# Performance work log

Measured on AMD Instinct MI355X. Metric: run time of the kernel, lower is better.

## Reference

```python
import jax, jax.numpy as jnp
import numpy as np

B, L, C = 8, 3136, 384
H_, W_ = 56, 56
WS, SS, NH = 7, 3, 12
HID, AD, SD = 1536, 16, 48  # mlp hidden, Bi_direct adapter dim, dim//scale_factor


def _rpi(w):
    # relative position index, [N, N] int
    coords = np.stack(np.meshgrid(np.arange(w), np.arange(w), indexing='ij')).reshape(2, -1)
    rc = (coords[:, :, None] - coords[:, None, :]).transpose(1, 2, 0)
    rc[:, :, 0] += w - 1
    rc[:, :, 1] += w - 1
    rc[:, :, 0] *= 2 * w - 1
    return rc.sum(-1)


def _shift_mask(Hp, Wp, w, s):
    # [nW, N, N] float mask with 0 / -100, as in the torch code
    img = np.zeros((1, Hp, Wp, 1), np.float32)
    cnt = 0
    sl = (slice(0, -w), slice(-w, -s), slice(-s, None))
    for h in sl:
        for v in sl:
            img[:, h, v, :] = cnt
            cnt += 1
    mw = img.reshape(1, Hp // w, w, Wp // w, w, 1).transpose(0, 1, 3, 2, 4, 5).reshape(-1, w * w)
    am = mw[:, None, :] - mw[:, :, None]
    return np.where(am != 0, np.float32(-100.0), np.float32(0.0))


def _ln(x, g, b, eps=1e-5):
    m = x.mean(-1, keepdims=True)
    v = ((x - m) ** 2).mean(-1, keepdims=True)
    return (x - m) * jax.lax.rsqrt(v + eps) * g + b


def _wpart(x, w):
    b, h, ww, c = x.shape
    return x.reshape(b, h // w, w, ww // w, w, c).transpose(0, 1, 3, 2, 4, 5).reshape(-1, w, w, c)


def _wrev(win, w, h, ww):
    b = win.shape[0] // (h * ww // w // w)
    return win.reshape(b, h // w, ww // w, w, w, -1).transpose(0, 1, 3, 2, 4, 5).reshape(b, h, ww, -1)


def _attn(xw, w_qkv, b_qkv, w_proj, b_proj, rpb, rpi, mask):
    B_, N, c = xw.shape
    d = c // NH
    scale = d ** -0.5
    qkv = (xw @ w_qkv + b_qkv).reshape(B_, N, 3, NH, d).transpose(2, 0, 3, 1, 4)
    q, k, v = qkv[0] * scale, qkv[1], qkv[2]  # [B_, NH, N, d]
    a = jnp.einsum('bhnd,bhmd->bhnm', q, k)
    bias = rpb[rpi.reshape(-1)].reshape(N, N, NH).transpose(2, 0, 1)
    a = a + bias[None]
    if mask is not None:
        nW = mask.shape[0]
        a = (a.reshape(B_ // nW, nW, NH, N, N) + mask[None, :, None]).reshape(B_, NH, N, N)
    a = jax.nn.softmax(a, axis=-1)
    out = jnp.einsum('bhnm,bhmd->bhnd', a, v).transpose(0, 2, 1, 3).reshape(B_, N, c)
    return out @ w_proj + b_proj


def setup_inputs() -> dict:
    key = jax.random.key(0)
    ks = iter(jax.random.split(key, 24))
    r = lambda shape: jax.random.normal(next(ks), shape, jnp.float32) * 0.02
    inp = dict(
        x_FMAG=jax.random.normal(next(ks), (B, L, C), jnp.float32),
        x=jax.random.normal(next(ks), (B, L, C), jnp.float32),
        z=jax.random.normal(next(ks), (B, L, C), jnp.float32),
        mask_z=1,
        ln1_g=jnp.ones(C), ln1_b=jnp.zeros(C),
        ln2_g=jnp.ones(C), ln2_b=jnp.zeros(C),
        w_qkv=r((C, 3 * C)), b_qkv=jnp.zeros(3 * C),
        w_proj=r((C, C)), b_proj=jnp.zeros(C),
        rpb=r(((2 * WS - 1) ** 2, NH)),
        w_fc1=r((C, HID)), b_fc1=jnp.zeros(HID),
        w_fc2=r((HID, C)), b_fc2=jnp.zeros(C),
        st_dw=r((C, SD)), st_db=jnp.zeros(SD), st_uw=r((SD, C)), st_ub=jnp.zeros(C),
        t_dw=r((C, AD)), t_db=jnp.zeros(AD), t_uw=r((AD, C)), t_ub=jnp.zeros(C),
        t2_dw=r((C, AD)), t2_db=jnp.zeros(AD), t2_uw=r((AD, C)), t2_ub=jnp.zeros(C),
    )
    return inp


def reference(x_FMAG, x, z, mask_z, ln1_g, ln1_b, ln2_g, ln2_b, w_qkv, b_qkv, w_proj, b_proj, rpb,
              w_fc1, b_fc1, w_fc2, b_fc2, st_dw, st_db, st_uw, st_ub,
              t_dw, t_db, t_uw, t_ub, t2_dw, t2_db, t2_uw, t2_ub):
    rpi = jnp.asarray(_rpi(WS))
    gelu = lambda y: jax.nn.gelu(y, approximate=False)
    # adapter_st (Single_adapter_s): bottleneck with GELU
    x = gelu(x_FMAG @ st_dw + st_db) @ st_uw + st_ub + x
    shortcut_x = x
    xn = _ln(x, ln1_g, ln1_b).reshape(B, H_, W_, C)
    # x branch: NO pre-shift (faithful to source), no mask, but rolled +shift after
    xw = _wpart(xn, WS).reshape(-1, WS * WS, C)
    awx = _attn(xw, w_qkv, b_qkv, w_proj, b_proj, rpb, rpi, None)
    awx4 = awx.reshape(-1, WS, WS, C)
    x = jnp.roll(_wrev(awx4, WS, H_, W_), (SS, SS), (1, 2)).reshape(B, L, C)
    # z branch: shifted, with shift attention mask (mask_z is not None)
    shortcut_z = z
    zn = _ln(z, ln1_g, ln1_b).reshape(B, H_, W_, C)
    sz = jnp.roll(zn, (-SS, -SS), (1, 2))
    mask = jnp.asarray(_shift_mask(H_, W_, WS, SS)) if mask_z else None
    zw = _wpart(sz, WS).reshape(-1, WS * WS, C)
    awz = _attn(zw, w_qkv, b_qkv, w_proj, b_proj, rpb, rpi, mask)
    awz4 = awz.reshape(-1, WS, WS, C)
    z = jnp.roll(_wrev(awz4, WS, H_, W_), (SS, SS), (1, 2)).reshape(B, L, C)
    # cross adapters (Bi_direct_adapter: linear down/up, no activation)
    ad_t = lambda y: (y @ t_dw + t_db) @ t_uw + t_ub
    ad_t2 = lambda y: (y @ t2_dw + t2_db) @ t2_uw + t2_ub
    x1 = shortcut_x + x + ad_t(shortcut_z)
    z1 = shortcut_z + z + ad_t(shortcut_x)
    mlp = lambda y: gelu(y @ w_fc1 + b_fc1) @ w_fc2 + b_fc2
    x2 = x1 + mlp(_ln(x1, ln2_g, ln2_b)) + ad_t2(z1)
    z2 = z1 + mlp(_ln(z1, ln2_g, ln2_b)) + ad_t2(x1)
    return (x2, awx4, z2, awz4)
```

## Files before the change

### kernel.cpp

```cpp
#include <hip/hip_runtime.h>
#include <hip/hip_bf16.h>


#define TOK 25088
#define TELEM 9633792L

typedef __attribute__((ext_vector_type(4))) float f32x4;
typedef __attribute__((ext_vector_type(8))) short bf16x8;
typedef __attribute__((address_space(3))) unsigned int as3_u32;
typedef __attribute__((address_space(1))) const unsigned int as1_u32;

__device__ __forceinline__ float ldc(const void* p, long i, int code, int bf) {
  if (code == 1 ? bf : (code == 2))
    return __bfloat162float(((const __hip_bfloat16*)p)[i]);
  return ((const float*)p)[i];
}
__device__ __forceinline__ void stAny(void* p, long i, int bf, float v) {
  if (bf) ((__hip_bfloat16*)p)[i] = __float2bfloat16(v);
  else ((float*)p)[i] = v;
}
__device__ __forceinline__ unsigned short f2b(float f) {
  __hip_bfloat16 h = __float2bfloat16(f);
  return *reinterpret_cast<unsigned short*>(&h);
}
__device__ __forceinline__ void ld8f(const void* p, long rowbase, int c,
                                     int code, int bf, float* o) {
  bool isb = (code == 1) ? (bf != 0) : (code == 2);
  if (isb) {
    bf16x8 v = *(const bf16x8*)((const __hip_bfloat16*)p + rowbase + c);
#pragma unroll
    for (int i = 0; i < 8; ++i)
      o[i] = __uint_as_float(((unsigned int)(unsigned short)v[i]) << 16);
  } else {
    const float* f = (const float*)p + rowbase + c;
#pragma unroll
    for (int i = 0; i < 8; ++i) o[i] = f[i];
  }
}
__device__ __forceinline__ void st8(void* p, long rowbase, int c, bool isb,
                                    const float* o) {
  if (isb) {
    bf16x8 v;
#pragma unroll
    for (int i = 0; i < 8; ++i) v[i] = (short)f2b(o[i]);
    *(bf16x8*)((__hip_bfloat16*)p + rowbase + c) = v;
  } else {
    float* f = (float*)p + rowbase + c;
#pragma unroll
    for (int i = 0; i < 8; ++i) f[i] = o[i];
  }
}

__global__ void detect_dtype(const unsigned int* __restrict__ w, int* flag) {
  __shared__ int cnt;
  if (threadIdx.x == 0) cnt = 0;
  __syncthreads();
  int local = 0;
  for (int i = threadIdx.x; i < 4096; i += blockDim.x) {
    unsigned int lo = w[i] & 0xFFFFu;
    unsigned int e = (lo >> 7) & 0xFFu;
    if ((e >= 100u && e <= 135u) || lo == 0u) local++;
  }
  atomicAdd(&cnt, local);
  __syncthreads();
  if (threadIdx.x == 0) *flag = (cnt > 2600) ? 1 : 0;
}

__global__ __launch_bounds__(256) void transpose_to_bf16(
    const void* __restrict__ in, __hip_bfloat16* __restrict__ out, int K,
    int N, const int* __restrict__ flagp) {
  int bf = *flagp;
  __shared__ float tile[32][33];
  int nb = blockIdx.x * 32, kb = blockIdx.y * 32;
  int tx = threadIdx.x & 31, ty = threadIdx.x >> 5;
#pragma unroll
  for (int r = 0; r < 32; r += 8)
    tile[ty + r][tx] = ldc(in, (long)(kb + ty + r) * N + nb + tx, 1, bf);
  __syncthreads();
#pragma unroll
  for (int r = 0; r < 32; r += 8)
    out[(long)(nb + ty + r) * K + kb + tx] = __float2bfloat16(tile[tx][ty + r]);
}

__global__ __launch_bounds__(256) void build_tab(const void* __restrict__ rpb,
                                                 float* __restrict__ tab,
                                                 const int* __restrict__ flagp) {
  int bf = *flagp;
  int idx = blockIdx.x * 256 + threadIdx.x;
  if (idx >= 48 * 2401) return;
  int m = idx % 49;
  int n = (idx / 49) % 49;
  int head = (idx / 2401) % 12;
  int cls = idx / (2401 * 12);
  int in_ = n / 7, jn = n % 7, im = m / 7, jm = m % 7;
  int ridx = (in_ - im + 6) * 13 + (jn - jm + 6);
  float v = ldc(rpb, (long)ridx * 12 + head, 1, bf);
  int whE = (cls >> 1) & 1, wwE = cls & 1;
  int rhn = whE ? (in_ < 4 ? 1 : 2) : 0;
  int rwn = wwE ? (jn < 4 ? 1 : 2) : 0;
  int rhm = whE ? (im < 4 ? 1 : 2) : 0;
  int rwm = wwE ? (jm < 4 ? 1 : 2) : 0;
  if ((rhn * 3 + rwn) != (rhm * 3 + rwm)) v -= 100.f;
  tab[idx] = v;
}

__global__ __launch_bounds__(512) void gemm_bf16(
    const __hip_bfloat16* __restrict__ A, const __hip_bfloat16* __restrict__ BT,
    const void* __restrict__ bias, void* __restrict__ C, int cmode, long coff,
    long coff2, long Msplit, int accum, int doGelu, int M, int N, int K,
    const int* __restrict__ flagp) {
  const int bf = *flagp;
  __shared__ __hip_bfloat16 As[2][256 * 32];
  __shared__ __hip_bfloat16 Bs[2][128 * 32];
  const int tid = threadIdx.x;
  const int lane = tid & 63, wave = tid >> 6;
  const int wr = wave >> 1, wc = wave & 1;

  const int gx = gridDim.x;
  long id = (long)blockIdx.y * gx + blockIdx.x;
  const long nwg = (long)gx * gridDim.y;
  {
    const long q = nwg >> 3, r = nwg & 7;
    const long xcd = id & 7, pos = id >> 3;
    id = (xcd < r) ? xcd * (q + 1) + pos : r * (q + 1) + (xcd - r) * q + pos;
  }
  const long m0 = (id / gx) * 256;
  const int n0 = (int)(id % gx) * 128;

  f32x4 acc[4][4] = {};

  const int srow = wave * 16 + (lane >> 2);
  const int scol = (lane & 3) * 8;
  const __hip_bfloat16* pA0 = A + (m0 + srow) * K + scol;
  const __hip_bfloat16* pB0 = BT + (long)(n0 + srow) * K + scol;
  const long rstepA = 128 * (long)K;
  const int ldsA0 = (wave * 16) * 32;
  const int ldsA1 = (128 + wave * 16) * 32;
  const int ldsB0 = (wave * 16) * 32;

  const int row = lane & 15;
  const int kk = (lane >> 4) * 8;
  const int nt = K / 32;

  auto stage = [&](int buf, int t) {
    const int k0 = t * 32;
    __builtin_amdgcn_global_load_lds((as1_u32*)(pA0 + k0),
                                     (as3_u32*)(&As[buf][ldsA0]), 16, 0, 0);
    __builtin_amdgcn_global_load_lds((as1_u32*)(pA0 + rstepA + k0),
                                     (as3_u32*)(&As[buf][ldsA1]), 16, 0, 0);
    __builtin_amdgcn_global_load_lds((as1_u32*)(pB0 + k0),
                                     (as3_u32*)(&Bs[buf][ldsB0]), 16, 0, 0);
  };

  stage(0, 0);
  if (nt > 1) {
    stage(1, 1);
    asm volatile("s_waitcnt vmcnt(3)" ::: "memory");
  } else {
    asm volatile("s_waitcnt vmcnt(0)" ::: "memory");
  }
  __builtin_amdgcn_sched_barrier(0);
  __builtin_amdgcn_s_barrier();

  for (int t = 0; t < nt; ++t) {
    const int cur = t & 1;
    bf16x8 af[4], bfr[4];
#pragma unroll
    for (int i = 0; i < 4; ++i)
      af[i] = *(const bf16x8*)(&As[cur][(wr * 64 + i * 16 + row) * 32 + kk]);
#pragma unroll
    for (int j = 0; j < 4; ++j)
      bfr[j] = *(const bf16x8*)(&Bs[cur][(wc * 64 + j * 16 + row) * 32 + kk]);
    asm volatile("s_waitcnt lgkmcnt(0)" ::: "memory");
    __builtin_amdgcn_sched_barrier(0);
    __builtin_amdgcn_s_barrier();
    if (t + 2 < nt) stage(cur, t + 2);
#pragma unroll
    for (int i = 0; i < 4; ++i)
#pragma unroll
      for (int j = 0; j < 4; ++j)
        acc[i][j] = __builtin_amdgcn_mfma_f32_16x16x32_bf16(af[i], bfr[j],
                                                            acc[i][j], 0, 0, 0);
    if (t + 1 < nt) {
      if (t + 2 < nt)
        asm volatile("s_waitcnt vmcnt(3)" ::: "memory");
      else
        asm volatile("s_waitcnt vmcnt(0)" ::: "memory");
      __builtin_amdgcn_sched_barrier(0);
      __builtin_amdgcn_s_barrier();
    }
  }

  const int crow = (lane >> 4) * 4;
  const int ccol = lane & 15;
#pragma unroll
  for (int i = 0; i < 4; ++i) {
#pragma unroll
    for (int r = 0; r < 4; ++r) {
      long m = m0 + wr * 64 + i * 16 + crow + r;
#pragma unroll
      for (int j = 0; j < 4; ++j) {
        int n = n0 + wc * 64 + j * 16 + ccol;
        float v = acc[i][j][r];
        if (bias) v += ldc(bias, n, 1, bf);
        if (doGelu) v = 0.5f * v * (1.f + erff(v * 0.70710678118f));
        long idx = m * (long)N + n;
        if (cmode == 0) {
          ((__hip_bfloat16*)C)[idx] = __float2bfloat16(v);
        } else {
          long odx = (m < Msplit) ? coff + idx
                                  : coff2 + (m - Msplit) * (long)N + n;
          if (accum) v += ldc(C, odx, 1, bf);
          stAny(C, odx, bf, v);
        }
      }
    }
  }
}

__global__ __launch_bounds__(256) void st_fused(
    const void* __restrict__ xF, const void* __restrict__ x_in,
    const void* __restrict__ dw, const void* __restrict__ db,
    const void* __restrict__ uw, const void* __restrict__ ub,
    __hip_bfloat16* __restrict__ out, const int* __restrict__ flagp) {
  const int bf = *flagp;
  __shared__ float Wd[48 * 384];
  __shared__ float Wu[48 * 384];
  __shared__ float Db[48], Ub[384];
  for (int i = threadIdx.x; i < 48 * 384; i += 256) {
    int k = i / 384, c = i % 384;
    Wd[i] = ldc(dw, (long)c * 48 + k, 1, bf);
    Wu[i] = ldc(uw, i, 1, bf);
  }
  for (int i = threadIdx.x; i < 48; i += 256) Db[i] = ldc(db, i, 1, bf);
  for (int i = threadIdx.x; i < 384; i += 256) Ub[i] = ldc(ub, i, 1, bf);
  __syncthreads();
  const long t = (long)blockIdx.x * 256 + threadIdx.x;
  float hid[48];
#pragma unroll
  for (int k = 0; k < 48; ++k) hid[k] = Db[k];
  for (int c = 0; c < 384; c += 8) {
    float x8[8];
    ld8f(xF, t * 384, c, 1, bf, x8);
    for (int k = 0; k < 48; ++k) {
      const float* w = &Wd[k * 384 + c];
      float s = 0.f;
#pragma unroll
      for (int i = 0; i < 8; ++i) s += x8[i] * w[i];
      hid[k] += s;
    }
  }
#pragma unroll
  for (int k = 0; k < 48; ++k) {
    float h = hid[k];
    hid[k] = 0.5f * h * (1.f + erff(h * 0.70710678118f));
  }
  for (int c = 0; c < 384; c += 8) {
    float o[8];
    ld8f(x_in, t * 384, c, 1, bf, o);
#pragma unroll
    for (int i = 0; i < 8; ++i) o[i] += Ub[c + i];
    for (int k = 0; k < 48; ++k) {
      const float* w = &Wu[k * 384 + c];
      float h = hid[k];
#pragma unroll
      for (int i = 0; i < 8; ++i) o[i] += h * w[i];
    }
    st8(out, t * 384, c, true, o);
  }
}

__global__ __launch_bounds__(256) void adapter_dual(
    const void* __restrict__ inA, int cA, const void* __restrict__ inB, int cB,
    const void* __restrict__ baseX, int cbX, const void* __restrict__ baseZ,
    int cbZ, const void* __restrict__ gat, long goffX, long goffZ,
    int doGather, const void* __restrict__ dw, const void* __restrict__ dbias,
    const void* __restrict__ uw, const void* __restrict__ ubias,
    void* __restrict__ outX, long ooffX, void* __restrict__ outZ, long ooffZ,
    int outRaw, const int* __restrict__ flagp) {
  const int bf = *flagp;
  __shared__ float Wd[16 * 384];
  __shared__ float Wu[16 * 384];
  __shared__ float Db[16], Ub[384];
  for (int i = threadIdx.x; i < 16 * 384; i += 256) {
    int k = i / 384, c = i % 384;
    Wd[i] = ldc(dw, (long)c * 16 + k, 1, bf);
    Wu[i] = ldc(uw, i, 1, bf);
  }
  if (threadIdx.x < 16) Db[threadIdx.x] = ldc(dbias, threadIdx.x, 1, bf);
  for (int i = threadIdx.x; i < 384; i += 256) Ub[i] = ldc(ubias, i, 1, bf);
  __syncthreads();
  const long t = (long)blockIdx.x * 256 + threadIdx.x;
  long grow = 0;
  if (doGather) {
    int b = (int)(t / 3136);
    int hw = (int)(t % 3136);
    int h = hw / 56, w = hw % 56;
    int hp = (h - 3 + 56) % 56, wp = (w - 3 + 56) % 56;
    int win = b * 64 + (hp / 7) * 8 + (wp / 7);
    int n = (hp % 7) * 7 + (wp % 7);
    grow = ((long)win * 49 + n) * 384;
  }
  float hidA[16], hidB[16];
#pragma unroll
  for (int k = 0; k < 16; ++k) {
    hidA[k] = Db[k];
    hidB[k] = Db[k];
  }
  for (int c = 0; c < 384; c += 8) {
    float a8[8], b8[8];
    ld8f(inA, t * 384, c, cA, bf, a8);
    ld8f(inB, t * 384, c, cB, bf, b8);
#pragma unroll
    for (int k = 0; k < 16; ++k) {
      const float* w = &Wd[k * 384 + c];
      float sa = 0.f, sb = 0.f;
#pragma unroll
      for (int i = 0; i < 8; ++i) {
        sa += a8[i] * w[i];
        sb += b8[i] * w[i];
      }
      hidA[k] += sa;
      hidB[k] += sb;
    }
  }
  const bool oisb = outRaw ? (bf != 0) : true;
  for (int c = 0; c < 384; c += 8) {
    float ox[8], oz[8];
    ld8f(baseX, t * 384, c, cbX, bf, ox);
    ld8f(baseZ, t * 384, c, cbZ, bf, oz);
    if (doGather) {
      float g[8];
      ld8f(gat, goffX + grow, c, 1, bf, g);
#pragma unroll
      for (int i = 0; i < 8; ++i) ox[i] += g[i];
      ld8f(gat, goffZ + grow, c, 1, bf, g);
#pragma unroll
      for (int i = 0; i < 8; ++i) oz[i] += g[i];
    }
#pragma unroll
    for (int i = 0; i < 8; ++i) {
      ox[i] += Ub[c + i];
      oz[i] += Ub[c + i];
    }
#pragma unroll
    for (int k = 0; k < 16; ++k) {
      const float* w = &Wu[k * 384 + c];
      float ha = hidA[k], hb = hidB[k];
#pragma unroll
      for (int i = 0; i < 8; ++i) {
        ox[i] += ha * w[i];
        oz[i] += hb * w[i];
      }
    }
    st8(outX, ooffX + t * 384, c, oisb, ox);
    st8(outZ, ooffZ + t * 384, c, oisb, oz);
  }
}

__global__ __launch_bounds__(128) void ln_kernel(
    const void* __restrict__ X, int xc, const void* __restrict__ g,
    const void* __restrict__ b, __hip_bfloat16* __restrict__ out,
    const int* __restrict__ flagp) {
  int bf = *flagp;
  long t = blockIdx.x;
  int tid = threadIdx.x;
  float v[3];
  float s = 0.f;
#pragma unroll
  for (int r = 0; r < 3; ++r) {
    v[r] = ldc(X, t * 384 + tid + r * 128, xc, bf);
    s += v[r];
  }
  __shared__ float red[2], red2[2];
  for (int off = 32; off; off >>= 1) s += __shfl_down(s, off, 64);
  if ((tid & 63) == 0) red[tid >> 6] = s;
  __syncthreads();
  float mean = (red[0] + red[1]) * (1.f / 384.f);
  float var = 0.f;
#pragma unroll
  for (int r = 0; r < 3; ++r) {
    float d = v[r] - mean;
    var += d * d;
  }
  for (int off = 32; off; off >>= 1) var += __shfl_down(var, off, 64);
  if ((tid & 63) == 0) red2[tid >> 6] = var;
  __syncthreads();
  float rstd = rsqrtf((red2[0] + red2[1]) * (1.f / 384.f) + 1e-5f);
#pragma unroll
  for (int r = 0; r < 3; ++r) {
    int c = tid + r * 128;
    out[t * 384 + c] = __float2bfloat16((v[r] - mean) * rstd *
                                        ldc(g, c, 1, bf) + ldc(b, c, 1, bf));
  }
}

__global__ __launch_bounds__(256) void attn_mfma(
    const __hip_bfloat16* __restrict__ qkv, const float* __restrict__ tab,
    __hip_bfloat16* __restrict__ outp, const int* __restrict__ maskz) {
  __shared__ __hip_bfloat16 lds[4][64 * 72 + 32 * 72];
  const int wave = threadIdx.x >> 6, lane = threadIdx.x & 63;
  const int pair = blockIdx.x * 4 + wave;
  const int head = pair % 12;
  const int win = pair / 12;
  const int shifted = win >= 512;
  const int wn = win & 511;
  const int b = wn >> 6, wh = (wn >> 3) & 7, ww = wn & 7;
  const int useMask = shifted && (*maskz != 0);
  const int cls = useMask ? (((wh == 7) ? 2 : 0) | ((ww == 7) ? 1 : 0)) : 0;
  const float* tb = tab + (long)(cls * 12 + head) * 2401;
  __hip_bfloat16* P = lds[wave];
  __hip_bfloat16* VT = lds[wave] + 64 * 72;

  auto tokOf = [&](int n) -> long {
    n = (n < 49) ? n : 0;
    int i = n / 7, j = n % 7;
    int h = wh * 7 + i, w = ww * 7 + j;
    if (shifted) {
      h = (h + 3) % 56;
      w = (w + 3) % 56;
    }
    return (shifted ? (long)TOK : 0) + ((long)b * 56 + h) * 56 + w;
  };

  const int fr = lane & 15;
  const int fq = lane >> 4;
  bf16x8 qf[4], kf[4];
#pragma unroll
  for (int i = 0; i < 4; ++i) {
    long t = tokOf(i * 16 + fr);
    const __hip_bfloat16* basep = qkv + t * 1152 + head * 32 + fq * 8;
    qf[i] = *(const bf16x8*)(basep);
    kf[i] = *(const bf16x8*)(basep + 384);
  }
  for (int e = lane; e < 32 * 16; e += 64)
    VT[(e >> 4) * 72 + 48 + (e & 15)] = __float2bfloat16(0.f);
  for (int e = lane; e < 49 * 32; e += 64) {
    int n = e >> 5, d = e & 31;
    VT[d * 72 + n] = qkv[tokOf(n) * 1152 + 768 + head * 32 + d];
  }
  f32x4 acc[4][4] = {};
#pragma unroll
  for (int i = 0; i < 4; ++i)
#pragma unroll
    for (int j = 0; j < 4; ++j)
      acc[i][j] =
          __builtin_amdgcn_mfma_f32_16x16x32_bf16(qf[i], kf[j], acc[i][j], 0, 0, 0);
  const float scale = 0.17677669529663687f;
#pragma unroll
  for (int i = 0; i < 4; ++i) {
#pragma unroll
    for (int r = 0; r < 4; ++r) {
      int n = i * 16 + fq * 4 + r;
      float s[4];
      float mx = -1e30f;
#pragma unroll
      for (int j = 0; j < 4; ++j) {
        int m = j * 16 + fr;
        float v = acc[i][j][r] * scale;
        if (m < 49 && n < 49) v += tb[n * 49 + m];
        s[j] = (m < 49) ? v : -1e30f;
        mx = fmaxf(mx, s[j]);
      }
#pragma unroll
      for (int d = 1; d < 16; d <<= 1) mx = fmaxf(mx, __shfl_xor(mx, d));
      float sum = 0.f;
#pragma unroll
      for (int j = 0; j < 4; ++j) {
        float p = (16 * j + fr < 49) ? __expf(s[j] - mx) : 0.f;
        s[j] = p;
        sum += p;
      }
#pragma unroll
      for (int d = 1; d < 16; d <<= 1) sum += __shfl_xor(sum, d);
      float inv = 1.f / sum;
#pragma unroll
      for (int j = 0; j < 4; ++j)
        P[n * 72 + j * 16 + fr] = __float2bfloat16(s[j] * inv);
    }
  }
  f32x4 o[4][2] = {};
#pragma unroll
  for (int ks = 0; ks < 2; ++ks) {
    bf16x8 pa[4], vb[2];
#pragma unroll
    for (int i2 = 0; i2 < 4; ++i2)
      pa[i2] = *(const bf16x8*)(P + (i2 * 16 + fr) * 72 + ks * 32 + fq * 8);
#pragma unroll
    for (int j2 = 0; j2 < 2; ++j2)
      vb[j2] = *(const bf16x8*)(VT + (j2 * 16 + fr) * 72 + ks * 32 + fq * 8);
#pragma unroll
    for (int i2 = 0; i2 < 4; ++i2)
#pragma unroll
      for (int j2 = 0; j2 < 2; ++j2)
        o[i2][j2] =
            __builtin_amdgcn_mfma_f32_16x16x32_bf16(pa[i2], vb[j2], o[i2][j2], 0, 0, 0);
  }
#pragma unroll
  for (int i2 = 0; i2 < 4; ++i2) {
#pragma unroll
    for (int r = 0; r < 4; ++r) {
      int n = i2 * 16 + fq * 4 + r;
      if (n < 49) {
#pragma unroll
        for (int j2 = 0; j2 < 2; ++j2)
          outp[((long)win * 49 + n) * 384 + head * 32 + j2 * 16 + fr] =
              __float2bfloat16(o[i2][j2][r]);
      }
    }
  }
}

extern "C" void kernel_launch(void* const* d_in, const int* in_sizes, int n_in,
                              void* d_out, int out_size, void* d_ws,
                              size_t ws_size, hipStream_t stream) {
  const void* x_FMAG = d_in[0];
  const void* x_in = d_in[1];
  const void* z_in = d_in[2];
  const int* mask_z = (const int*)d_in[3];
  const void* ln1_g = d_in[4];
  const void* ln1_b = d_in[5];
  const void* ln2_g = d_in[6];
  const void* ln2_b = d_in[7];
  const void* w_qkv = d_in[8];
  const void* b_qkv = d_in[9];
  const void* w_proj = d_in[10];
  const void* b_proj = d_in[11];
  const void* rpb = d_in[12];
  const void* w_fc1 = d_in[13];
  const void* b_fc1 = d_in[14];
  const void* w_fc2 = d_in[15];
  const void* b_fc2 = d_in[16];
  const void* st_dw = d_in[17];
  const void* st_db = d_in[18];
  const void* st_uw = d_in[19];
  const void* st_ub = d_in[20];
  const void* t_dw = d_in[21];
  const void* t_db = d_in[22];
  const void* t_uw = d_in[23];
  const void* t_ub = d_in[24];
  const void* t2_dw = d_in[25];
  const void* t2_db = d_in[26];
  const void* t2_uw = d_in[27];
  const void* t2_ub = d_in[28];

  const long T = TELEM;
  char* base = (char*)d_ws;
  __hip_bfloat16* W6bf = (__hip_bfloat16*)base; base += T * 2;
  __hip_bfloat16* W7bf = (__hip_bfloat16*)base; base += T * 2;
  __hip_bfloat16* Sbf = (__hip_bfloat16*)base; base += 2 * T * 2;
  char* D = base; base += 16 * T;
  __hip_bfloat16* W0bf = (__hip_bfloat16*)D;
  __hip_bfloat16* QKVbf = (__hip_bfloat16*)(D + 2 * T);
  __hip_bfloat16* Hbf = (__hip_bfloat16*)D;
  __hip_bfloat16* TQ = (__hip_bfloat16*)base; base += 384L * 1152 * 2;
  __hip_bfloat16* TP = (__hip_bfloat16*)base; base += 384L * 384 * 2;
  __hip_bfloat16* T1 = (__hip_bfloat16*)base; base += 384L * 1536 * 2;
  __hip_bfloat16* T2 = (__hip_bfloat16*)base; base += 1536L * 384 * 2;
  float* tab = (float*)base; base += 48L * 2401 * 4;
  int* flag = (int*)base;

  detect_dtype<<<1, 256, 0, stream>>>((const unsigned int*)x_FMAG, flag);

  transpose_to_bf16<<<dim3(1152 / 32, 384 / 32), 256, 0, stream>>>(
      w_qkv, TQ, 384, 1152, flag);
  transpose_to_bf16<<<dim3(384 / 32, 384 / 32), 256, 0, stream>>>(
      w_proj, TP, 384, 384, flag);
  transpose_to_bf16<<<dim3(1536 / 32, 384 / 32), 256, 0, stream>>>(
      w_fc1, T1, 384, 1536, flag);
  transpose_to_bf16<<<dim3(384 / 32, 1536 / 32), 256, 0, stream>>>(
      w_fc2, T2, 1536, 384, flag);
  build_tab<<<(48 * 2401 + 255) / 256, 256, 0, stream>>>(rpb, tab, flag);

  auto gemmb = [&](const __hip_bfloat16* A, const __hip_bfloat16* BT,
                   const void* bias, void* C, int cmode, long coff, long coff2,
                   long msplit, int accum, int gelu, int M, int N, int K) {
    dim3 g(N / 128, M / 256);
    gemm_bf16<<<g, 512, 0, stream>>>(A, BT, bias, C, cmode, coff, coff2,
                                     msplit, accum, gelu, M, N, K, flag);
  };

  st_fused<<<TOK / 256, 256, 0, stream>>>(x_FMAG, x_in, st_dw, st_db, st_uw,
                                          st_ub, W0bf, flag);
  ln_kernel<<<TOK, 128, 0, stream>>>(W0bf, 2, ln1_g, ln1_b, Sbf, flag);
  ln_kernel<<<TOK, 128, 0, stream>>>(z_in, 1, ln1_g, ln1_b, Sbf + T, flag);
  gemmb(Sbf, TQ, b_qkv, QKVbf, 0, 0, 0, 2 * TOK, 0, 0, 2 * TOK, 1152, 384);
  attn_mfma<<<1024 * 12 / 4, 256, 0, stream>>>(QKVbf, tab, Sbf, mask_z);
  gemmb(Sbf, TP, b_proj, d_out, 1, T, 3 * T, TOK, 0, 0, 2 * TOK, 384, 384);
  adapter_dual<<<TOK / 256, 256, 0, stream>>>(
      z_in, 1, W0bf, 2, W0bf, 2, z_in, 1, d_out, T, 3 * T, 1, t_dw, t_db,
      t_uw, t_ub, W6bf, 0, W7bf, 0, 0, flag);
  ln_kernel<<<TOK, 128, 0, stream>>>(W6bf, 2, ln2_g, ln2_b, Sbf, flag);
  ln_kernel<<<TOK, 128, 0, stream>>>(W7bf, 2, ln2_g, ln2_b, Sbf + T, flag);
  gemmb(Sbf, T1, b_fc1, Hbf, 0, 0, 0, 2 * TOK, 0, 1, 2 * TOK, 1536, 384);
  adapter_dual<<<TOK / 256, 256, 0, stream>>>(
      W7bf, 2, W6bf, 2, W6bf, 2, W7bf, 2, nullptr, 0, 0, 0, t2_dw, t2_db,
      t2_uw, t2_ub, d_out, 0, d_out, 2 * T, 1, flag);
  gemmb(Hbf, T2, b_fc2, d_out, 1, 0, 2 * T, TOK, 1, 0, 2 * TOK, 384, 1536);
}
```

Measured before the change: 1.296 ms.

## Split adapter kernels into down/up passes with multi-thread-per-token work split

The fused adapter and scale-token kernels, which used one thread per token and launched only 98 blocks, are each split into a down-projection kernel and an up-projection kernel. The hidden activations go through small fp32 global buffers. Each token is now handled by 8 or 16 threads, giving many more blocks and better occupancy. Shared-memory weights are stored as bf16, which halves LDS use. The cost is extra launches, a global round trip for the hidden vectors, and bf16 rounding of the weights.

```diff
diff --git a/kernel.cpp b/kernel.cpp
--- a/kernel.cpp
+++ b/kernel.cpp
@@ -22,6 +22,9 @@
 __device__ __forceinline__ unsigned short f2b(float f) {
   __hip_bfloat16 h = __float2bfloat16(f);
   return *reinterpret_cast<unsigned short*>(&h);
+}
+__device__ __forceinline__ float b2f(short s) {
+  return __uint_as_float(((unsigned int)(unsigned short)s) << 16);
 }
 __device__ __forceinline__ void ld8f(const void* p, long rowbase, int c,
                                      int code, int bf, float* o) {
@@ -29,8 +32,7 @@
   if (isb) {
     bf16x8 v = *(const bf16x8*)((const __hip_bfloat16*)p + rowbase + c);
 #pragma unroll
-    for (int i = 0; i < 8; ++i)
-      o[i] = __uint_as_float(((unsigned int)(unsigned short)v[i]) << 16);
+    for (int i = 0; i < 8; ++i) o[i] = b2f(v[i]);
   } else {
     const float* f = (const float*)p + rowbase + c;
 #pragma unroll
@@ -218,79 +220,139 @@
   }
 }
 
-__global__ __launch_bounds__(256) void st_fused(
-    const void* __restrict__ xF, const void* __restrict__ x_in,
-    const void* __restrict__ dw, const void* __restrict__ db,
+__global__ __launch_bounds__(256) void st_down(
+    const void* __restrict__ xF, const void* __restrict__ dw,
+    const void* __restrict__ db, float* __restrict__ hid,
+    const int* __restrict__ flagp) {
+  const int bf = *flagp;
+  __shared__ __hip_bfloat16 Wd[48 * 384];
+  __shared__ float Db[48];
+  for (int i = threadIdx.x; i < 48 * 384; i += 256) {
+    int k = i / 384, c = i % 384;
+    Wd[i] = __float2bfloat16(ldc(dw, (long)c * 48 + k, 1, bf));
+  }
+  if (threadIdx.x < 48) Db[threadIdx.x] = ldc(db, threadIdx.x, 1, bf);
+  __syncthreads();
+  const long t = (long)blockIdx.x * 32 + (threadIdx.x >> 3);
+  const int kg = (threadIdx.x & 7) * 6;
+  float acc[6];
+#pragma unroll
+  for (int k = 0; k < 6; ++k) acc[k] = Db[kg + k];
+  for (int c = 0; c < 384; c += 8) {
+    float x8[8];
+    ld8f(xF, t * 384, c, 1, bf, x8);
+#pragma unroll
+    for (int k = 0; k < 6; ++k) {
+      bf16x8 w = *(const bf16x8*)(&Wd[(kg + k) * 384 + c]);
+      float s = 0.f;
+#pragma unroll
+      for (int i = 0; i < 8; ++i) s += x8[i] * b2f(w[i]);
+      acc[k] += s;
+    }
+  }
+#pragma unroll
+  for (int k = 0; k < 6; ++k) {
+    float h = acc[k];
+    hid[t * 48 + kg + k] = 0.5f * h * (1.f + erff(h * 0.70710678118f));
+  }
+}
+
+__global__ __launch_bounds__(256) void st_up(
+    const void* __restrict__ x_in, const float* __restrict__ hid,
     const void* __restrict__ uw, const void* __restrict__ ub,
     __hip_bfloat16* __restrict__ out, const int* __restrict__ flagp) {
   const int bf = *flagp;
-  __shared__ float Wd[48 * 384];
-  __shared__ float Wu[48 * 384];
-  __shared__ float Db[48], Ub[384];
-  for (int i = threadIdx.x; i < 48 * 384; i += 256) {
+  __shared__ __hip_bfloat16 Wu[48 * 384];
+  __shared__ float Ub[384];
+  for (int i = threadIdx.x; i < 48 * 384; i += 256)
+    Wu[i] = __float2bfloat16(ldc(uw, i, 1, bf));
+  for (int i = threadIdx.x; i < 384; i += 256) Ub[i] = ldc(ub, i, 1, bf);
+  __syncthreads();
+  const long t = (long)blockIdx.x * 16 + (threadIdx.x >> 4);
+  const int c0 = (threadIdx.x & 15) * 24;
+  float acc[24];
+#pragma unroll
+  for (int i = 0; i < 24; ++i) acc[i] = Ub[c0 + i];
+#pragma unroll
+  for (int b3 = 0; b3 < 3; ++b3) {
+    float x8[8];
+    ld8f(x_in, t * 384, c0 + b3 * 8, 1, bf, x8);
+#pragma unroll
+    for (int i = 0; i < 8; ++i) acc[b3 * 8 + i] += x8[i];
+  }
+  const float* hrow = hid + t * 48;
+  for (int k = 0; k < 48; ++k) {
+    float h = hrow[k];
+#pragma unroll
+    for (int b3 = 0; b3 < 3; ++b3) {
+      bf16x8 w = *(const bf16x8*)(&Wu[k * 384 + c0 + b3 * 8]);
+#pragma unroll
+      for (int i = 0; i < 8; ++i) acc[b3 * 8 + i] += h * b2f(w[i]);
+    }
+  }
+#pragma unroll
+  for (int b3 = 0; b3 < 3; ++b3) st8(out, t * 384, c0 + b3 * 8, true, acc + b3 * 8);
+}
+
+__global__ __launch_bounds__(256) void ad_down(
+    const void* __restrict__ inA, int cA, const void* __restrict__ inB, int cB,
+    const void* __restrict__ dw, const void* __restrict__ dbias,
+    float* __restrict__ hidA, float* __restrict__ hidB,
+    const int* __restrict__ flagp) {
+  const int bf = *flagp;
+  __shared__ __hip_bfloat16 Wd[16 * 384];
+  __shared__ float Db[16];
+  for (int i = threadIdx.x; i < 16 * 384; i += 256) {
     int k = i / 384, c = i % 384;
-    Wd[i] = ldc(dw, (long)c * 48 + k, 1, bf);
-    Wu[i] = ldc(uw, i, 1, bf);
-  }
-  for (int i = threadIdx.x; i < 48; i += 256) Db[i] = ldc(db, i, 1, bf);
-  for (int i = threadIdx.x; i < 384; i += 256) Ub[i] = ldc(ub, i, 1, bf);
-  __syncthreads();
-  const long t = (long)blockIdx.x * 256 + threadIdx.x;
-  float hid[48];
-#pragma unroll
-  for (int k = 0; k < 48; ++k) hid[k] = Db[k];
+    Wd[i] = __float2bfloat16(ldc(dw, (long)c * 16 + k, 1, bf));
+  }
+  if (threadIdx.x < 16) Db[threadIdx.x] = ldc(dbias, threadIdx.x, 1, bf);
+  __syncthreads();
+  const long t = (long)blockIdx.x * 32 + (threadIdx.x >> 3);
+  const int kg = (threadIdx.x & 7) * 2;
+  float aA[2] = {Db[kg], Db[kg + 1]};
+  float aB[2] = {Db[kg], Db[kg + 1]};
   for (int c = 0; c < 384; c += 8) {
-    float x8[8];
-    ld8f(xF, t * 384, c, 1, bf, x8);
-    for (int k = 0; k < 48; ++k) {
-      const float* w = &Wd[k * 384 + c];
-      float s = 0.f;
-#pragma unroll
-      for (int i = 0; i < 8; ++i) s += x8[i] * w[i];
-      hid[k] += s;
-    }
-  }
-#pragma unroll
-  for (int k = 0; k < 48; ++k) {
-    float h = hid[k];
-    hid[k] = 0.5f * h * (1.f + erff(h * 0.70710678118f));
-  }
-  for (int c = 0; c < 384; c += 8) {
-    float o[8];
-    ld8f(x_in, t * 384, c, 1, bf, o);
-#pragma unroll
-    for (int i = 0; i < 8; ++i) o[i] += Ub[c + i];
-    for (int k = 0; k < 48; ++k) {
-      const float* w = &Wu[k * 384 + c];
-      float h = hid[k];
-#pragma unroll
-      for (int i = 0; i < 8; ++i) o[i] += h * w[i];
-    }
-    st8(out, t * 384, c, true, o);
-  }
-}
-
-__global__ __launch_bounds__(256) void adapter_dual(
-    const void* __restrict__ inA, int cA, const void* __restrict__ inB, int cB,
+    float a8[8], b8[8];
+    ld8f(inA, t * 384, c, cA, bf, a8);
+    ld8f(inB, t * 384, c, cB, bf, b8);
+#pragma unroll
+    for (int k = 0; k < 2; ++k) {
+      bf16x8 w = *(const bf16x8*)(&Wd[(kg + k) * 384 + c]);
+      float sa = 0.f, sb = 0.f;
+#pragma unroll
+      for (int i = 0; i < 8; ++i) {
+        float wf = b2f(w[i]);
+        sa += a8[i] * wf;
+        sb += b8[i] * wf;
+      }
+      aA[k] += sa;
+      aB[k] += sb;
+    }
+  }
+#pragma unroll
+  for (int k = 0; k < 2; ++k) {
+    hidA[t * 16 + kg + k] = aA[k];
+    hidB[t * 16 + kg + k] = aB[k];
+  }
+}
+
+__global__ __launch_bounds__(256) void ad_up(
+    const float* __restrict__ hidA, const float* __restrict__ hidB,
     const void* __restrict__ baseX, int cbX, const void* __restrict__ baseZ,
     int cbZ, const void* __restrict__ gat, long goffX, long goffZ,
-    int doGather, const void* __restrict__ dw, const void* __restrict__ dbias,
-    const void* __restrict__ uw, const void* __restrict__ ubias,
+    int doGather, const void* __restrict__ uw, const void* __restrict__ ubias,
     void* __restrict__ outX, long ooffX, void* __restrict__ outZ, long ooffZ,
     int outRaw, const int* __restrict__ flagp) {
   const int bf = *flagp;
-  __shared__ float Wd[16 * 384];
-  __shared__ float Wu[16 * 384];
-  __shared__ float Db[16], Ub[384];
-  for (int i = threadIdx.x; i < 16 * 384; i += 256) {
-    int k = i / 384, c = i % 384;
-    Wd[i] = ldc(dw, (long)c * 16 + k, 1, bf);
-    Wu[i] = ldc(uw, i, 1, bf);
-  }
-  if (threadIdx.x < 16) Db[threadIdx.x] = ldc(dbias, threadIdx.x, 1, bf);
+  __shared__ __hip_bfloat16 Wu[16 * 384];
+  __shared__ float Ub[384];
+  for (int i = threadIdx.x; i < 16 * 384; i += 256)
+    Wu[i] = __float2bfloat16(ldc(uw, i, 1, bf));
   for (int i = threadIdx.x; i < 384; i += 256) Ub[i] = ldc(ubias, i, 1, bf);
   __syncthreads();
-  const long t = (long)blockIdx.x * 256 + threadIdx.x;
+  const long t = (long)blockIdx.x * 16 + (threadIdx.x >> 4);
+  const int c0 = (threadIdx.x & 15) * 24;
   long grow = 0;
   if (doGather) {
     int b = (int)(t / 3136);
@@ -301,60 +363,54 @@
     int n = (hp % 7) * 7 + (wp % 7);
     grow = ((long)win * 49 + n) * 384;
   }
-  float hidA[16], hidB[16];
-#pragma unroll
+  float ox[24], oz[24];
+#pragma unroll
+  for (int i = 0; i < 24; ++i) {
+    ox[i] = Ub[c0 + i];
+    oz[i] = Ub[c0 + i];
+  }
+#pragma unroll
+  for (int b3 = 0; b3 < 3; ++b3) {
+    float v8[8];
+    ld8f(baseX, t * 384, c0 + b3 * 8, cbX, bf, v8);
+#pragma unroll
+    for (int i = 0; i < 8; ++i) ox[b3 * 8 + i] += v8[i];
+    ld8f(baseZ, t * 384, c0 + b3 * 8, cbZ, bf, v8);
+#pragma unroll
+    for (int i = 0; i < 8; ++i) oz[b3 * 8 + i] += v8[i];
+  }
+  if (doGather) {
+#pragma unroll
+    for (int b3 = 0; b3 < 3; ++b3) {
+      float g8[8];
+      ld8f(gat, goffX + grow, c0 + b3 * 8, 1, bf, g8);
+#pragma unroll
+      for (int i = 0; i < 8; ++i) ox[b3 * 8 + i] += g8[i];
+      ld8f(gat, goffZ + grow, c0 + b3 * 8, 1, bf, g8);
+#pragma unroll
+      for (int i = 0; i < 8; ++i) oz[b3 * 8 + i] += g8[i];
+    }
+  }
+  const float* ha = hidA + t * 16;
+  const float* hb = hidB + t * 16;
   for (int k = 0; k < 16; ++k) {
-    hidA[k] = Db[k];
-    hidB[k] = Db[k];
-  }
-  for (int c = 0; c < 384; c += 8) {
-    float a8[8], b8[8];
-    ld8f(inA, t * 384, c, cA, bf, a8);
-    ld8f(inB, t * 384, c, cB, bf, b8);
-#pragma unroll
-    for (int k = 0; k < 16; ++k) {
-      const float* w = &Wd[k * 384 + c];
-      float sa = 0.f, sb = 0.f;
+    float hA = ha[k], hB = hb[k];
+#pragma unroll
+    for (int b3 = 0; b3 < 3; ++b3) {
+      bf16x8 w = *(const bf16x8*)(&Wu[k * 384 + c0 + b3 * 8]);
 #pragma unroll
       for (int i = 0; i < 8; ++i) {
-        sa += a8[i] * w[i];
-        sb += b8[i] * w[i];
+        float wf = b2f(w[i]);
+        ox[b3 * 8 + i] += hA * wf;
+        oz[b3 * 8 + i] += hB * wf;
       }
-      hidA[k] += sa;
-      hidB[k] += sb;
     }
   }
   const bool oisb = outRaw ? (bf != 0) : true;
-  for (int c = 0; c < 384; c += 8) {
-    float ox[8], oz[8];
-    ld8f(baseX, t * 384, c, cbX, bf, ox);
-    ld8f(baseZ, t * 384, c, cbZ, bf, oz);
-    if (doGather) {
-      float g[8];
-      ld8f(gat, goffX + grow, c, 1, bf, g);
-#pragma unroll
-      for (int i = 0; i < 8; ++i) ox[i] += g[i];
-      ld8f(gat, goffZ + grow, c, 1, bf, g);
-#pragma unroll
-      for (int i = 0; i < 8; ++i) oz[i] += g[i];
-    }
-#pragma unroll
-    for (int i = 0; i < 8; ++i) {
-      ox[i] += Ub[c + i];
-      oz[i] += Ub[c + i];
-    }
-#pragma unroll
-    for (int k = 0; k < 16; ++k) {
-      const float* w = &Wu[k * 384 + c];
-      float ha = hidA[k], hb = hidB[k];
-#pragma unroll
-      for (int i = 0; i < 8; ++i) {
-        ox[i] += ha * w[i];
-        oz[i] += hb * w[i];
-      }
-    }
-    st8(outX, ooffX + t * 384, c, oisb, ox);
-    st8(outZ, ooffZ + t * 384, c, oisb, oz);
+#pragma unroll
+  for (int b3 = 0; b3 < 3; ++b3) {
+    st8(outX, ooffX + t * 384, c0 + b3 * 8, oisb, ox + b3 * 8);
+    st8(outZ, ooffZ + t * 384, c0 + b3 * 8, oisb, oz + b3 * 8);
   }
 }
 
@@ -558,6 +614,9 @@
   __hip_bfloat16* T1 = (__hip_bfloat16*)base; base += 384L * 1536 * 2;
   __hip_bfloat16* T2 = (__hip_bfloat16*)base; base += 1536L * 384 * 2;
   float* tab = (float*)base; base += 48L * 2401 * 4;
+  float* hidS = (float*)base; base += (long)TOK * 48 * 4;
+  float* hidA = (float*)base; base += (long)TOK * 16 * 4;
+  float* hidB = (float*)base; base += (long)TOK * 16 * 4;
   int* flag = (int*)base;
 
   detect_dtype<<<1, 256, 0, stream>>>((const unsigned int*)x_FMAG, flag);
@@ -580,21 +639,25 @@
                                      msplit, accum, gelu, M, N, K, flag);
   };
 
-  st_fused<<<TOK / 256, 256, 0, stream>>>(x_FMAG, x_in, st_dw, st_db, st_uw,
-                                          st_ub, W0bf, flag);
+  st_down<<<TOK / 32, 256, 0, stream>>>(x_FMAG, st_dw, st_db, hidS, flag);
+  st_up<<<TOK / 16, 256, 0, stream>>>(x_in, hidS, st_uw, st_ub, W0bf, flag);
   ln_kernel<<<TOK, 128, 0, stream>>>(W0bf, 2, ln1_g, ln1_b, Sbf, flag);
   ln_kernel<<<TOK, 128, 0, stream>>>(z_in, 1, ln1_g, ln1_b, Sbf + T, flag);
   gemmb(Sbf, TQ, b_qkv, QKVbf, 0, 0, 0, 2 * TOK, 0, 0, 2 * TOK, 1152, 384);
   attn_mfma<<<1024 * 12 / 4, 256, 0, stream>>>(QKVbf, tab, Sbf, mask_z);
   gemmb(Sbf, TP, b_proj, d_out, 1, T, 3 * T, TOK, 0, 0, 2 * TOK, 384, 384);
-  adapter_dual<<<TOK / 256, 256, 0, stream>>>(
-      z_in, 1, W0bf, 2, W0bf, 2, z_in, 1, d_out, T, 3 * T, 1, t_dw, t_db,
-      t_uw, t_ub, W6bf, 0, W7bf, 0, 0, flag);
+  ad_down<<<TOK / 32, 256, 0, stream>>>(z_in, 1, W0bf, 2, t_dw, t_db, hidA,
+                                        hidB, flag);
+  ad_up<<<TOK / 16, 256, 0, stream>>>(hidA, hidB, W0bf, 2, z_in, 1, d_out, T,
+                                      3 * T, 1, t_uw, t_ub, W6bf, 0, W7bf, 0,
+                                      0, flag);
   ln_kernel<<<TOK, 128, 0, stream>>>(W6bf, 2, ln2_g, ln2_b, Sbf, flag);
   ln_kernel<<<TOK, 128, 0, stream>>>(W7bf, 2, ln2_g, ln2_b, Sbf + T, flag);
   gemmb(Sbf, T1, b_fc1, Hbf, 0, 0, 0, 2 * TOK, 0, 1, 2 * TOK, 1536, 384);
-  adapter_dual<<<TOK / 256, 256, 0, stream>>>(
-      W7bf, 2, W6bf, 2, W6bf, 2, W7bf, 2, nullptr, 0, 0, 0, t2_dw, t2_db,
-      t2_uw, t2_ub, d_out, 0, d_out, 2 * T, 1, flag);
+  ad_down<<<TOK / 32, 256, 0, stream>>>(W7bf, 2, W6bf, 2, t2_dw, t2_db, hidA,
+                                        hidB, flag);
+  ad_up<<<TOK / 16, 256, 0, stream>>>(hidA, hidB, W6bf, 2, W7bf, 2, nullptr,
+                                      0, 0, 0, t2_uw, t2_ub, d_out, 0, d_out,
+                                      2 * T, 1, flag);
   gemmb(Hbf, T2, b_fc2, d_out, 1, 0, 2 * T, TOK, 1, 0, 2 * TOK, 384, 1536);
 }
```

New measurement: 1.206 ms. 1.07x faster.
